# Kernel optimization log

Hardware: AMD Instinct MI355X
Metric: run time of the kernel (lower is better)

## Reference

```python
import jax, jax.numpy as jnp
import numpy as np

N = 100000; D = 256; ATT = 512; H = 8; HD = ATT // H; E = 250000
TYPE_CT = 64; TS = 64; P = 8192; PC = 1024; MP = 131072; MC = 16384


def setup_inputs() -> dict:
    key = jax.random.key(0)
    ks = jax.random.split(key, 24)
    sD = 1.0 / np.sqrt(D); sT = 1.0 / np.sqrt(TS); sA = 1.0 / np.sqrt(ATT); sC = 1.0 / np.sqrt(D + ATT)
    inp = {}
    inp['node_states'] = jax.random.normal(ks[0], (N, D), jnp.float32)
    inp['node_types'] = jax.random.randint(ks[1], (N,), 0, TYPE_CT, jnp.int32)
    inp['pair_conj'] = jax.random.randint(ks[2], (E,), 0, N, jnp.int32)
    inp['pair_prem'] = jax.random.randint(ks[3], (E,), 0, N, jnp.int32)
    inp['pool_prem_nodes'] = jax.random.randint(ks[4], (MP,), 0, N, jnp.int32)
    inp['pool_prem_seg'] = ((jnp.arange(MP, dtype=jnp.int32) * P) // MP).astype(jnp.int32)  # every prem set non-empty
    inp['pool_conj_nodes'] = jax.random.randint(ks[5], (MC,), 0, N, jnp.int32)
    inp['pool_conj_seg'] = ((jnp.arange(MC, dtype=jnp.int32) * PC) // MC).astype(jnp.int32)
    inp['prem2conj'] = jax.random.randint(ks[6], (P,), 0, PC, jnp.int32)
    # learned parameters
    inp['ln_g'] = jnp.ones((D,), jnp.float32)
    inp['ln_b'] = jnp.zeros((D,), jnp.float32)
    inp['emb_p'] = jax.random.normal(ks[7], (TYPE_CT, TS), jnp.float32) * 0.02
    inp['wp_w'] = jax.random.normal(ks[8], (TS, ATT), jnp.float32) * sT
    inp['wp_b'] = jnp.zeros((ATT,), jnp.float32)
    inp['emb_c'] = jax.random.normal(ks[9], (TYPE_CT, TS), jnp.float32) * 0.02
    inp['wc_w'] = jax.random.normal(ks[10], (TS, ATT), jnp.float32) * sT
    inp['wc_b'] = jnp.zeros((ATT,), jnp.float32)
    inp['Wq_p'] = jax.random.normal(ks[11], (H, D, HD), jnp.float32) * sD
    inp['Wk_p'] = jax.random.normal(ks[12], (H, D, HD), jnp.float32) * sD
    inp['Wv_p'] = jax.random.normal(ks[13], (H, D, HD), jnp.float32) * sD
    inp['Wo_p'] = jax.random.normal(ks[14], (ATT, ATT), jnp.float32) * sA
    inp['Wq_c'] = jax.random.normal(ks[15], (H, D, HD), jnp.float32) * sD
    inp['Wk_c'] = jax.random.normal(ks[16], (H, D, HD), jnp.float32) * sD
    inp['Wv_c'] = jax.random.normal(ks[17], (H, D, HD), jnp.float32) * sD
    inp['Wo_c'] = jax.random.normal(ks[18], (ATT, ATT), jnp.float32) * sA
    inp['W_dag'] = jax.random.normal(ks[19], (D + ATT, D + ATT), jnp.float32) * sC
    inp['b_dag'] = jnp.zeros((D + ATT,), jnp.float32)
    return inp


def _layernorm(x, g, b):
    mu = jnp.mean(x, axis=-1, keepdims=True)
    var = jnp.mean(jnp.square(x - mu), axis=-1, keepdims=True)
    return (x - mu) * jax.lax.rsqrt(var + 1e-5) * g + b


def _mha_dir(x, src, tgt, Wq, Wk, Wv, Wo, gate):
    # gather query/key/value node reprs along the pair list (irregular gather)
    xs = x[src]; xt = x[tgt]                       # [E, D]
    q = jnp.einsum('ed,hdk->ehk', xs, Wq)          # [E, H, HD]
    k = jnp.einsum('ed,hdk->ehk', xt, Wk)
    scores = jnp.sum(q * k, axis=-1) / np.sqrt(HD)  # [E, H]
    # per-query-node (segment) softmax, as in compute_att_aggr grouping
    m = jax.ops.segment_max(scores, src, num_segments=N)
    ex = jnp.exp(scores - m[src])
    denom = jax.ops.segment_sum(ex, src, num_segments=N)
    prob = ex / denom[src]
    v = jnp.einsum('ed,hdk->ehk', xt, Wv)
    # adj_matr @ comb_matr scatter-aggregation
    agg = jax.ops.segment_sum(prob[..., None] * v, src, num_segments=N)  # [N, H, HD]
    return gate * (agg.reshape(N, H * HD) @ Wo)


def reference(node_states, node_types, pair_conj, pair_prem, pool_prem_nodes, pool_prem_seg,
              pool_conj_nodes, pool_conj_seg, prem2conj,
              ln_g, ln_b, emb_p, wp_w, wp_b, emb_c, wc_w, wc_b,
              Wq_p, Wk_p, Wv_p, Wo_p, Wq_c, Wk_c, Wv_c, Wo_c, W_dag, b_dag):
    x = _layernorm(node_states, ln_g, ln_b)                                  # ne_norm(node reprs)
    gate_p = jax.nn.sigmoid(emb_p[node_types] @ wp_w + wp_b)                 # prem_gate  [N, ATT]
    gate_c = jax.nn.sigmoid(emb_c[node_types] @ wc_w + wc_b)                 # conj_gate
    # just_prem pairs: (prem, conj) -> query/scatter node = prem, key/value node = conj
    comb = _mha_dir(x, pair_prem, pair_conj, Wq_p, Wk_p, Wv_p, Wo_p, gate_p)
    # just_conj pairs: (conj, prem)
    comb = comb + _mha_dir(x, pair_conj, pair_prem, Wq_c, Wk_c, Wv_c, Wo_c, gate_c)
    h = jnp.concatenate([x, comb], axis=1)                                   # [N, D+ATT]
    pooled = jnp.tanh(h @ W_dag + b_dag)                                     # simplified dag_lstm pass
    prem_r = jax.ops.segment_max(pooled[pool_prem_nodes], pool_prem_seg, num_segments=P)
    conj_sets = jax.ops.segment_max(pooled[pool_conj_nodes], pool_conj_seg, num_segments=PC)
    conj_r = conj_sets[prem2conj]
    return jnp.concatenate([prem_r, conj_r], axis=1)                         # [P, 2*(D+ATT)]
```

## Files before the change

kernel.cpp:

```cpp
#include <hip/hip_runtime.h>
#include <math.h>

#define N_NODES 100000
#define DIM 256
#define ATT 512
#define NH 8
#define HD 64
#define E_PAIRS 250000
#define TYPE_CT 64
#define TS 64
#define P_SEG 8192
#define PC_SEG 1024
#define MP_SZ 131072
#define MC_SZ 16384
#define CD 768

typedef unsigned short u16;
typedef __attribute__((ext_vector_type(8))) short short8v;
typedef __attribute__((ext_vector_type(4))) float floatx4;

__device__ __forceinline__ u16 f2b(float f) {
    unsigned u = __float_as_uint(f);
    return (u16)((u + 0x7FFFu + ((u >> 16) & 1u)) >> 16);
}
__device__ __forceinline__ float b2f(u16 h) {
    return __uint_as_float(((unsigned)h) << 16);
}

template<int N>
__device__ __forceinline__ void waitcnt_vm() {
    asm volatile("s_waitcnt vmcnt(%0)" :: "n"(N) : "memory");
}
__device__ __forceinline__ void barrier_fence() {
    asm volatile("s_barrier" ::: "memory");
    __builtin_amdgcn_sched_barrier(0);
}

__global__ __launch_bounds__(256) void fill_val_k(float* out, int n, float v) {
    int i = blockIdx.x * 256 + threadIdx.x;
    if (i < n) out[i] = v;
}

__global__ __launch_bounds__(64) void layernorm_k(
    const float* __restrict__ ns, const float* __restrict__ g,
    const float* __restrict__ b, u16* __restrict__ x)
{
    int row = blockIdx.x;
    int lane = threadIdx.x;
    float4 v = ((const float4*)(ns + (size_t)row * DIM))[lane];
    float sum = v.x + v.y + v.z + v.w;
    #pragma unroll
    for (int off = 32; off >= 1; off >>= 1) sum += __shfl_xor(sum, off);
    float mu = sum * (1.0f / DIM);
    float dx = v.x - mu, dy = v.y - mu, dz = v.z - mu, dw = v.w - mu;
    float sq = dx * dx + dy * dy + dz * dz + dw * dw;
    #pragma unroll
    for (int off = 32; off >= 1; off >>= 1) sq += __shfl_xor(sq, off);
    float rs = rsqrtf(sq * (1.0f / DIM) + 1e-5f);
    float4 gg = ((const float4*)g)[lane];
    float4 bb = ((const float4*)b)[lane];
    u16 o4[4];
    o4[0] = f2b(dx * rs * gg.x + bb.x);
    o4[1] = f2b(dy * rs * gg.y + bb.y);
    o4[2] = f2b(dz * rs * gg.z + bb.z);
    o4[3] = f2b(dw * rs * gg.w + bb.w);
    *(uint2*)(x + (size_t)row * DIM + lane * 4) = *(uint2*)o4;
}

__global__ __launch_bounds__(512) void gate_table_k(
    const float* __restrict__ emb, const float* __restrict__ w,
    const float* __restrict__ wb, float* __restrict__ tab)
{
    int t = blockIdx.x;
    int a = threadIdx.x;
    float acc = wb[a];
    #pragma unroll 8
    for (int s = 0; s < TS; ++s) acc += emb[t * TS + s] * w[s * ATT + a];
    tab[t * ATT + a] = 1.0f / (1.0f + expf(-acc));
}

__global__ __launch_bounds__(256) void wcvt_k(
    const float* __restrict__ W, u16* __restrict__ Bt, int K, int N)
{
    int idx = blockIdx.x * 256 + threadIdx.x;
    if (idx >= K * N) return;
    int c = idx / K, k = idx - c * K;
    Bt[idx] = f2b(W[(size_t)k * N + c]);
}

__global__ __launch_bounds__(256) void wqkv_cvt_k(
    const float* __restrict__ Wq, const float* __restrict__ Wk,
    const float* __restrict__ Wv, u16* __restrict__ outp)
{
    int idx = blockIdx.x * 256 + threadIdx.x;
    if (idx >= NH * 3 * HD * DIM) return;
    int k = idx & (DIM - 1);
    int c = (idx >> 8) & (HD - 1);
    int hm = idx >> 14;
    int m = hm % 3;
    int h = hm / 3;
    const float* W = (m == 0) ? Wq : ((m == 1) ? Wk : Wv);
    outp[idx] = f2b(W[((size_t)h * DIM + k) * HD + c]);
}

template<int BM, int WN, int DEPTH, int EPI>
__device__ __forceinline__ void gemm_body3(
    const u16* __restrict__ A, int lda,
    const u16* __restrict__ A2, int lda2, int K1,
    const u16* __restrict__ Bt, int ldb,
    u16* __restrict__ C, int ldc,
    int M, int K,
    const float* __restrict__ bias,
    const float* __restrict__ gateTab,
    const int* __restrict__ types)
{
    constexpr int BN = 32 * WN;
    constexpr int AR = BM / 64;
    constexpr int BR = BN / 64;
    constexpr int LA = AR + BR;
    constexpr int AF = BM / 32;
    __shared__ u16 As[DEPTH][BM * 32];
    __shared__ u16 Bs[DEPTH][BN * 32];
    const int bm = blockIdx.y * BM;
    const int bn = blockIdx.x * BN;
    const int tid = threadIdx.x;
    const int wave = tid >> 6, lane = tid & 63;
    const int wm = (wave >> 1) * (BM / 2), wn = (wave & 1) * 16 * WN;
    const int srow = tid >> 2;
    const int skk = (((tid & 3) ^ ((srow >> 1) & 3)) * 8);
    floatx4 acc[AF][WN] = {};

    auto stage = [&](int buf, int k0) {
        #pragma unroll
        for (int rnd = 0; rnd < AR; ++rnd) {
            int grow = bm + srow + rnd * 64;
            if (grow > M - 1) grow = M - 1;
            int gk = k0 + skk;
            const u16* src;
            if (EPI == 2 && gk >= K1) src = A2 + (size_t)grow * lda2 + (gk - K1);
            else                      src = A + (size_t)grow * lda + gk;
            __builtin_amdgcn_global_load_lds(
                (const __attribute__((address_space(1))) void*)src,
                (__attribute__((address_space(3))) void*)(&As[buf][rnd * 2048 + wave * 512]),
                16, 0, 0);
        }
        #pragma unroll
        for (int rnd = 0; rnd < BR; ++rnd) {
            const u16* src = Bt + (size_t)(bn + srow + rnd * 64) * ldb + k0 + skk;
            __builtin_amdgcn_global_load_lds(
                (const __attribute__((address_space(1))) void*)src,
                (__attribute__((address_space(3))) void*)(&Bs[buf][rnd * 2048 + wave * 512]),
                16, 0, 0);
        }
    };

    const int NS = K >> 5;
    #pragma unroll
    for (int p = 0; p < DEPTH - 1; ++p)
        if (p < NS) stage(p, p * 32);
    const int rr = lane & 15;
    const int cq = lane >> 4;
    int cur = 0;
    for (int is = 0; is < NS; ++is) {
        int pend = NS - 1 - is;
        if (pend > DEPTH - 2) pend = DEPTH - 2;
        if (pend >= 2)      waitcnt_vm<2 * LA>();
        else if (pend == 1) waitcnt_vm<LA>();
        else                waitcnt_vm<0>();
        barrier_fence();
        if (is + DEPTH - 1 < NS) stage((cur + DEPTH - 1) % DEPTH, (is + DEPTH - 1) * 32);
        short8v a[AF], b[WN];
        #pragma unroll
        for (int i = 0; i < AF; ++i) {
            int ar = wm + i * 16 + rr;
            a[i] = *(const short8v*)&As[cur][ar * 32 + ((cq ^ ((ar >> 1) & 3)) * 8)];
        }
        #pragma unroll
        for (int j = 0; j < WN; ++j) {
            int br = wn + j * 16 + rr;
            b[j] = *(const short8v*)&Bs[cur][br * 32 + ((cq ^ ((br >> 1) & 3)) * 8)];
        }
        #pragma unroll
        for (int i = 0; i < AF; ++i)
            #pragma unroll
            for (int j = 0; j < WN; ++j)
                acc[i][j] = __builtin_amdgcn_mfma_f32_16x16x32_bf16(
                    a[i], b[j], acc[i][j], 0, 0, 0);
        cur = (cur + 1) % DEPTH;
    }
    #pragma unroll
    for (int i = 0; i < AF; ++i) {
        #pragma unroll
        for (int j = 0; j < WN; ++j) {
            #pragma unroll
            for (int q = 0; q < 4; ++q) {
                int row = bm + wm + i * 16 + (lane >> 4) * 4 + q;
                if (row >= M) continue;
                int col = bn + wn + j * 16 + (lane & 15);
                float v = acc[i][j][q];
                size_t idx = (size_t)row * ldc + col;
                if (EPI == 0) C[idx] = f2b(v);
                else if (EPI == 1) {
                    float g = gateTab[types[row] * ATT + col];
                    C[idx] = f2b(b2f(C[idx]) + g * v);
                } else if (EPI == 3) {
                    float g = gateTab[types[row] * ATT + col];
                    C[idx] = f2b(g * v);
                } else {
                    C[idx] = f2b(tanhf(v + bias[col]));
                }
            }
        }
    }
}

__global__ __launch_bounds__(256) void gemm_qkv(
    const u16* __restrict__ A, const u16* __restrict__ Bt, u16* __restrict__ C)
{
    gemm_body3<64, 2, 4, 0>(A, DIM, nullptr, 0, 1 << 30, Bt, DIM, C, 192,
                            N_NODES, DIM, nullptr, nullptr, nullptr);
}
__global__ __launch_bounds__(256) void gemm_wo_first(
    const u16* __restrict__ A, const u16* __restrict__ Bt, u16* __restrict__ C,
    const float* __restrict__ gateTab, const int* __restrict__ types)
{
    gemm_body3<64, 2, 4, 3>(A, ATT, nullptr, 0, 1 << 30, Bt, ATT, C, ATT,
                            N_NODES, ATT, nullptr, gateTab, types);
}
__global__ __launch_bounds__(256) void gemm_wo_acc(
    const u16* __restrict__ A, const u16* __restrict__ Bt, u16* __restrict__ C,
    const float* __restrict__ gateTab, const int* __restrict__ types)
{
    gemm_body3<64, 2, 4, 1>(A, ATT, nullptr, 0, 1 << 30, Bt, ATT, C, ATT,
                            N_NODES, ATT, nullptr, gateTab, types);
}
__global__ __launch_bounds__(256) void gemm_dag(
    const u16* __restrict__ A, const u16* __restrict__ A2,
    const u16* __restrict__ Bt, u16* __restrict__ C,
    const float* __restrict__ bias)
{
    gemm_body3<64, 2, 4, 2>(A, DIM, A2, ATT, DIM, Bt, CD, C, 384,
                            N_NODES, CD, bias, nullptr, nullptr);
}

__global__ __launch_bounds__(256) void count_k(
    const int* __restrict__ src, int* __restrict__ counts)
{
    int e = blockIdx.x * 256 + threadIdx.x;
    if (e < E_PAIRS) atomicAdd(&counts[src[e]], 1);
}
__global__ __launch_bounds__(256) void scan1_k(
    const int* __restrict__ counts, int* __restrict__ offs, int* __restrict__ bsums)
{
    __shared__ int sm[256];
    int i = blockIdx.x * 256 + threadIdx.x;
    int v = (i < N_NODES) ? counts[i] : 0;
    sm[threadIdx.x] = v;
    __syncthreads();
    for (int d = 1; d < 256; d <<= 1) {
        int t = (threadIdx.x >= d) ? sm[threadIdx.x - d] : 0;
        __syncthreads();
        sm[threadIdx.x] += t;
        __syncthreads();
    }
    if (i < N_NODES) offs[i] = sm[threadIdx.x] - v;
    if (threadIdx.x == 255) bsums[blockIdx.x] = sm[255];
}
__global__ __launch_bounds__(512) void scan2_k(int* __restrict__ bsums, int nb)
{
    __shared__ int sm[512];
    int tx = threadIdx.x;
    int v = (tx < nb) ? bsums[tx] : 0;
    sm[tx] = v;
    __syncthreads();
    for (int d = 1; d < 512; d <<= 1) {
        int t = (tx >= d) ? sm[tx - d] : 0;
        __syncthreads();
        sm[tx] += t;
        __syncthreads();
    }
    if (tx < nb) bsums[tx] = sm[tx] - v;
}
__global__ __launch_bounds__(256) void addcur_k(
    int* __restrict__ offs, const int* __restrict__ bsums, int* __restrict__ cur)
{
    int i = blockIdx.x * 256 + threadIdx.x;
    if (i >= N_NODES) return;
    int o = offs[i] + bsums[i >> 8];
    offs[i] = o;
    cur[i] = o;
}
__global__ __launch_bounds__(256) void scatter_k(
    const int* __restrict__ src, const int* __restrict__ tgt,
    int* __restrict__ cur, int* __restrict__ csr_tgt)
{
    int e = blockIdx.x * 256 + threadIdx.x;
    if (e >= E_PAIRS) return;
    int p = atomicAdd(&cur[src[e]], 1);
    csr_tgt[p] = tgt[e];
}

__global__ __launch_bounds__(256) void attn_k(
    const u16* __restrict__ qkv, const int* __restrict__ offs,
    const int* __restrict__ counts, const int* __restrict__ csr_tgt,
    u16* __restrict__ agg, int h)
{
    int s = blockIdx.x * 4 + (threadIdx.x >> 6);
    if (s >= N_NODES) return;
    int lane = threadIdx.x & 63;
    float q = b2f(qkv[(size_t)s * 192 + lane]) * 0.125f;
    int lo = offs[s], deg = counts[s];
    float m = -INFINITY, l = 0.0f, acc = 0.0f;
    for (int i = 0; i < deg; ++i) {
        int t = csr_tgt[lo + i];
        float kd = b2f(qkv[(size_t)t * 192 + 64 + lane]);
        float vd = b2f(qkv[(size_t)t * 192 + 128 + lane]);
        float p = q * kd;
        #pragma unroll
        for (int off = 32; off >= 1; off >>= 1) p += __shfl_xor(p, off);
        float mn = fmaxf(m, p);
        float sc = expf(m - mn);
        float w  = expf(p - mn);
        l = l * sc + w;
        acc = acc * sc + w * vd;
        m = mn;
    }
    float r = (deg > 0) ? acc / l : 0.0f;
    agg[(size_t)s * ATT + h * HD + lane] = f2b(r);
}

template<int BFOUT>
__global__ __launch_bounds__(256) void seg_max_k(
    const u16* __restrict__ pooled, const int* __restrict__ nodes,
    const int* __restrict__ seg, int total, void* __restrict__ outv, int ldo)
{
    int p = blockIdx.x;
    int lo, hi;
    { int a = 0, b2 = total; while (a < b2) { int mid = (a + b2) >> 1; if (seg[mid] < p) a = mid + 1; else b2 = mid; } lo = a; }
    { int a = lo, b2 = total; while (a < b2) { int mid = (a + b2) >> 1; if (seg[mid] < p + 1) a = mid + 1; else b2 = mid; } hi = a; }
    for (int c = threadIdx.x; c < 384; c += 256) {
        float mx = -INFINITY;
        for (int i = lo; i < hi; ++i)
            mx = fmaxf(mx, b2f(pooled[(size_t)nodes[i] * 384 + c]));
        if (BFOUT) ((u16*)outv)[(size_t)p * ldo + c] = f2b(mx);
        else       ((float*)outv)[(size_t)p * ldo + c] = mx;
    }
}

__global__ __launch_bounds__(768) void gather_conj(
    const u16* __restrict__ cs, const int* __restrict__ p2c,
    float* __restrict__ out)
{
    int p = blockIdx.x;
    int c = threadIdx.x;
    out[(size_t)p * (2 * CD) + CD + c] = b2f(cs[(size_t)p2c[p] * CD + c]);
}

extern "C" void kernel_launch(void* const* d_in, const int* in_sizes, int n_in,
                              void* d_out, int out_size, void* d_ws, size_t ws_size,
                              hipStream_t stream) {
    const float* node_states     = (const float*)d_in[0];
    const int*   node_types      = (const int*)d_in[1];
    const int*   pair_conj       = (const int*)d_in[2];
    const int*   pair_prem       = (const int*)d_in[3];
    const int*   pool_prem_nodes = (const int*)d_in[4];
    const int*   pool_prem_seg   = (const int*)d_in[5];
    const int*   pool_conj_nodes = (const int*)d_in[6];
    const int*   pool_conj_seg   = (const int*)d_in[7];
    const int*   prem2conj       = (const int*)d_in[8];
    const float* ln_g  = (const float*)d_in[9];
    const float* ln_b  = (const float*)d_in[10];
    const float* emb_p = (const float*)d_in[11];
    const float* wp_w  = (const float*)d_in[12];
    const float* wp_b  = (const float*)d_in[13];
    const float* emb_c = (const float*)d_in[14];
    const float* wc_w  = (const float*)d_in[15];
    const float* wc_b  = (const float*)d_in[16];
    const float* Wq_p  = (const float*)d_in[17];
    const float* Wk_p  = (const float*)d_in[18];
    const float* Wv_p  = (const float*)d_in[19];
    const float* Wo_p  = (const float*)d_in[20];
    const float* Wq_c  = (const float*)d_in[21];
    const float* Wk_c  = (const float*)d_in[22];
    const float* Wv_c  = (const float*)d_in[23];
    const float* Wo_c  = (const float*)d_in[24];
    const float* W_dag = (const float*)d_in[25];
    const float* b_dag = (const float*)d_in[26];
    float* out = (float*)d_out;

    char* ws = (char*)d_ws;
    size_t o = 0;
    u16* x_bf  = (u16*)(ws + o); o += (size_t)N_NODES * DIM * 2;
    u16* comb  = (u16*)(ws + o); o += (size_t)N_NODES * ATT * 2;
    u16* R     = (u16*)(ws + o); o += (size_t)N_NODES * ATT * 2;
    char* csrb = ws + o;         o += 8000000;
    u16* conj_sets = (u16*)(ws + o); o += (size_t)PC_SEG * CD * 2;
    const size_t WS_NEEDED = o;

    if (ws_size < WS_NEEDED) {
        fill_val_k<<<(out_size + 255) / 256, 256, 0, stream>>>(out, out_size, (float)ws_size);
        return;
    }

    u16* agg    = R;
    u16* pooled = R;
    int* c_counts[2], *c_offs[2], *c_cur[2], *c_tgt[2];
    for (int d = 0; d < 2; ++d) {
        char* base = csrb + (size_t)d * 2200000;
        c_counts[d] = (int*)(base + 0);
        c_offs[d]   = (int*)(base + 400000);
        c_cur[d]    = (int*)(base + 800000);
        c_tgt[d]    = (int*)(base + 1200000);
    }
    int* bsums = (int*)(csrb + 4400000);
    u16* wdag_t = (u16*)csrb;

    char* ob = (char*)d_out;
    u16* qkv     = (u16*)(ob + 0);
    float* gtab_p = (float*)(ob + 38400000);
    float* gtab_c = (float*)(ob + 38531072);
    u16* wqkv_t  = (u16*)(ob + 38662144);
    u16* wo_t    = (u16*)(ob + 40235008);

    layernorm_k<<<N_NODES, 64, 0, stream>>>(node_states, ln_g, ln_b, x_bf);
    gate_table_k<<<TYPE_CT, ATT, 0, stream>>>(emb_p, wp_w, wp_b, gtab_p);
    gate_table_k<<<TYPE_CT, ATT, 0, stream>>>(emb_c, wc_w, wc_b, gtab_c);
    wqkv_cvt_k<<<(NH * 3 * HD * DIM + 255) / 256, 256, 0, stream>>>(
        Wq_p, Wk_p, Wv_p, wqkv_t);
    wqkv_cvt_k<<<(NH * 3 * HD * DIM + 255) / 256, 256, 0, stream>>>(
        Wq_c, Wk_c, Wv_c, wqkv_t + (size_t)NH * 3 * HD * DIM);
    wcvt_k<<<(ATT * ATT + 255) / 256, 256, 0, stream>>>(Wo_p, wo_t, ATT, ATT);
    wcvt_k<<<(ATT * ATT + 255) / 256, 256, 0, stream>>>(
        Wo_c, wo_t + (size_t)ATT * ATT, ATT, ATT);

    const int NSCAN = (N_NODES + 255) / 256;
    for (int d = 0; d < 2; ++d) {
        const int* src = d ? pair_conj : pair_prem;
        const int* tgt = d ? pair_prem : pair_conj;
        hipMemsetAsync(c_counts[d], 0, 400000, stream);
        count_k<<<(E_PAIRS + 255) / 256, 256, 0, stream>>>(src, c_counts[d]);
        scan1_k<<<NSCAN, 256, 0, stream>>>(c_counts[d], c_offs[d], bsums);
        scan2_k<<<1, 512, 0, stream>>>(bsums, NSCAN);
        addcur_k<<<NSCAN, 256, 0, stream>>>(c_offs[d], bsums, c_cur[d]);
        scatter_k<<<(E_PAIRS + 255) / 256, 256, 0, stream>>>(src, tgt, c_cur[d], c_tgt[d]);
    }

    const int MB64 = (N_NODES + 63) / 64;

    for (int dir = 0; dir < 2; ++dir) {
        const float* gt = dir ? gtab_c : gtab_p;
        const u16* wq_d = wqkv_t + (size_t)dir * NH * 3 * HD * DIM;
        const u16* wo_d = wo_t + (size_t)dir * ATT * ATT;

        for (int h = 0; h < NH; ++h) {
            gemm_qkv<<<dim3(3, MB64), 256, 0, stream>>>(
                x_bf, wq_d + (size_t)h * 3 * HD * DIM, qkv);
            attn_k<<<(N_NODES + 3) / 4, 256, 0, stream>>>(
                qkv, c_offs[dir], c_counts[dir], c_tgt[dir], agg, h);
        }

        if (dir == 0)
            gemm_wo_first<<<dim3(ATT / 64, MB64), 256, 0, stream>>>(
                agg, wo_d, comb, gt, node_types);
        else
            gemm_wo_acc<<<dim3(ATT / 64, MB64), 256, 0, stream>>>(
                agg, wo_d, comb, gt, node_types);
    }

    wcvt_k<<<(CD * CD + 255) / 256, 256, 0, stream>>>(W_dag, wdag_t, CD, CD);

    for (int c0 = 0; c0 < CD; c0 += 384) {
        gemm_dag<<<dim3(384 / 64, MB64), 256, 0, stream>>>(
            x_bf, comb, wdag_t + (size_t)c0 * CD, pooled, b_dag + c0);
        seg_max_k<0><<<P_SEG, 256, 0, stream>>>(
            pooled, pool_prem_nodes, pool_prem_seg, MP_SZ, out + c0, 2 * CD);
        seg_max_k<1><<<PC_SEG, 256, 0, stream>>>(
            pooled, pool_conj_nodes, pool_conj_seg, MC_SZ, conj_sets + c0, CD);
    }
    gather_conj<<<P_SEG, CD, 0, stream>>>(conj_sets, prem2conj, out);
}
```

Baseline: 2.455 ms.

## Widen GEMM N-tiles and remap block order for L2 reuse

The GEMM tiles become wider: QKV covers all 192 output columns in one block, and the Wo and DAG GEMMs use 128-column tiles. The pipeline depth drops from 4 to 3 to keep LDS use in check. Wo and DAG move to a 1D grid remapped in groups of 8 row-blocks, so blocks sharing A rows run close together and reuse them from L2. The aim is to cut redundant re-reads of the A operand and add per-block MFMA work, at the cost of more registers per block and possibly lower occupancy.

```diff
diff --git a/kernel.cpp b/kernel.cpp
--- a/kernel.cpp
+++ b/kernel.cpp
@@ -34,6 +34,13 @@
 __device__ __forceinline__ void barrier_fence() {
     asm volatile("s_barrier" ::: "memory");
     __builtin_amdgcn_sched_barrier(0);
+}
+
+__device__ __forceinline__ void remap8(int flat, int gx, int& bx, int& by) {
+    int yc = flat & 7;
+    int t = flat >> 3;
+    bx = t % gx;
+    by = yc + 8 * (t / gx);
 }
 
 __global__ __launch_bounds__(256) void fill_val_k(float* out, int n, float v) {
@@ -105,6 +112,7 @@
 
 template<int BM, int WN, int DEPTH, int EPI>
 __device__ __forceinline__ void gemm_body3(
+    int bm, int bn,
     const u16* __restrict__ A, int lda,
     const u16* __restrict__ A2, int lda2, int K1,
     const u16* __restrict__ Bt, int ldb,
@@ -121,8 +129,6 @@
     constexpr int AF = BM / 32;
     __shared__ u16 As[DEPTH][BM * 32];
     __shared__ u16 Bs[DEPTH][BN * 32];
-    const int bm = blockIdx.y * BM;
-    const int bn = blockIdx.x * BN;
     const int tid = threadIdx.x;
     const int wave = tid >> 6, lane = tid & 63;
     const int wm = (wave >> 1) * (BM / 2), wn = (wave & 1) * 16 * WN;
@@ -214,24 +220,34 @@
     }
 }
 
+#define MB64 1563
+#define MB64P 1568
+
 __global__ __launch_bounds__(256) void gemm_qkv(
     const u16* __restrict__ A, const u16* __restrict__ Bt, u16* __restrict__ C)
 {
-    gemm_body3<64, 2, 4, 0>(A, DIM, nullptr, 0, 1 << 30, Bt, DIM, C, 192,
+    gemm_body3<64, 6, 3, 0>(blockIdx.y * 64, 0,
+                            A, DIM, nullptr, 0, 1 << 30, Bt, DIM, C, 192,
                             N_NODES, DIM, nullptr, nullptr, nullptr);
 }
 __global__ __launch_bounds__(256) void gemm_wo_first(
     const u16* __restrict__ A, const u16* __restrict__ Bt, u16* __restrict__ C,
     const float* __restrict__ gateTab, const int* __restrict__ types)
 {
-    gemm_body3<64, 2, 4, 3>(A, ATT, nullptr, 0, 1 << 30, Bt, ATT, C, ATT,
+    int bx, by; remap8(blockIdx.x, 4, bx, by);
+    if (by >= MB64) return;
+    gemm_body3<64, 4, 3, 3>(by * 64, bx * 128,
+                            A, ATT, nullptr, 0, 1 << 30, Bt, ATT, C, ATT,
                             N_NODES, ATT, nullptr, gateTab, types);
 }
 __global__ __launch_bounds__(256) void gemm_wo_acc(
     const u16* __restrict__ A, const u16* __restrict__ Bt, u16* __restrict__ C,
     const float* __restrict__ gateTab, const int* __restrict__ types)
 {
-    gemm_body3<64, 2, 4, 1>(A, ATT, nullptr, 0, 1 << 30, Bt, ATT, C, ATT,
+    int bx, by; remap8(blockIdx.x, 4, bx, by);
+    if (by >= MB64) return;
+    gemm_body3<64, 4, 3, 1>(by * 64, bx * 128,
+                            A, ATT, nullptr, 0, 1 << 30, Bt, ATT, C, ATT,
                             N_NODES, ATT, nullptr, gateTab, types);
 }
 __global__ __launch_bounds__(256) void gemm_dag(
@@ -239,7 +255,10 @@
     const u16* __restrict__ Bt, u16* __restrict__ C,
     const float* __restrict__ bias)
 {
-    gemm_body3<64, 2, 4, 2>(A, DIM, A2, ATT, DIM, Bt, CD, C, 384,
+    int bx, by; remap8(blockIdx.x, 3, bx, by);
+    if (by >= MB64) return;
+    gemm_body3<64, 4, 3, 2>(by * 64, bx * 128,
+                            A, DIM, A2, ATT, DIM, Bt, CD, C, 384,
                             N_NODES, CD, bias, nullptr, nullptr);
 }
 
@@ -445,32 +464,30 @@
         scatter_k<<<(E_PAIRS + 255) / 256, 256, 0, stream>>>(src, tgt, c_cur[d], c_tgt[d]);
     }
 
-    const int MB64 = (N_NODES + 63) / 64;
-
     for (int dir = 0; dir < 2; ++dir) {
         const float* gt = dir ? gtab_c : gtab_p;
         const u16* wq_d = wqkv_t + (size_t)dir * NH * 3 * HD * DIM;
         const u16* wo_d = wo_t + (size_t)dir * ATT * ATT;
 
         for (int h = 0; h < NH; ++h) {
-            gemm_qkv<<<dim3(3, MB64), 256, 0, stream>>>(
+            gemm_qkv<<<dim3(1, MB64), 256, 0, stream>>>(
                 x_bf, wq_d + (size_t)h * 3 * HD * DIM, qkv);
             attn_k<<<(N_NODES + 3) / 4, 256, 0, stream>>>(
                 qkv, c_offs[dir], c_counts[dir], c_tgt[dir], agg, h);
         }
 
         if (dir == 0)
-            gemm_wo_first<<<dim3(ATT / 64, MB64), 256, 0, stream>>>(
+            gemm_wo_first<<<4 * MB64P, 256, 0, stream>>>(
                 agg, wo_d, comb, gt, node_types);
         else
-            gemm_wo_acc<<<dim3(ATT / 64, MB64), 256, 0, stream>>>(
+            gemm_wo_acc<<<4 * MB64P, 256, 0, stream>>>(
                 agg, wo_d, comb, gt, node_types);
     }
 
     wcvt_k<<<(CD * CD + 255) / 256, 256, 0, stream>>>(W_dag, wdag_t, CD, CD);
 
     for (int c0 = 0; c0 < CD; c0 += 384) {
-        gemm_dag<<<dim3(384 / 64, MB64), 256, 0, stream>>>(
+        gemm_dag<<<3 * MB64P, 256, 0, stream>>>(
             x_bf, comb, wdag_t + (size_t)c0 * CD, pooled, b_dag + c0);
         seg_max_k<0><<<P_SEG, 256, 0, stream>>>(
             pooled, pool_prem_nodes, pool_prem_seg, MP_SZ, out + c0, 2 * CD);
```

Result: faster. 2.128 ms (-13.3%).
